# Optimization experiments

Hardware: AMD Instinct MI355X
Metric: run time of the kernel (lower is better)

Reference implementation:

```python
import jax, jax.numpy as jnp
import numpy as np

ALPHA = 0.2  # LeakyReLU negative slope


def setup_inputs() -> dict:
    key = jax.random.key(0)
    k1, k2, k3 = jax.random.split(key, 3)
    B, N, F_IN, F_OUT = 8, 2048, 128, 64
    h = jax.random.normal(k1, (B, N, F_IN), dtype=jnp.float32)
    # nn.Linear(in, out, bias=False).weight is [out, in]; we store the transposed
    # matmul-ready form W: [F_IN, F_OUT].
    W = jax.random.normal(k2, (F_IN, F_OUT), dtype=jnp.float32) * 0.05
    # attn_fc: Linear(2*F_OUT, 1, bias=False) -> weight vector a: [2*F_OUT]
    a = jax.random.normal(k3, (2 * F_OUT,), dtype=jnp.float32) * 0.05
    return {"h": h, "W": W, "a": a}


def reference(h, W, a):
    # h: [B, N, F_in], W: [F_in, F_out], a: [2*F_out]
    F_out = W.shape[1]
    Wh = h @ W  # [B, N, F_out]
    # cat([Wh_i, Wh_j]) @ a == Wh_i @ a1 + Wh_j @ a2 -- identical math,
    # avoids materializing the [B, N, N, 2F] tensor.
    s_i = Wh @ a[:F_out]  # [B, N] contribution of row node i
    s_j = Wh @ a[F_out:]  # [B, N] contribution of col node j
    e = jax.nn.leaky_relu(s_i[:, :, None] + s_j[:, None, :], negative_slope=ALPHA)  # [B, N, N]
    attn = jax.nn.softmax(e, axis=-1)  # softmax over neighbors j
    h_prime = jnp.einsum('bij,bjf->bif', attn, Wh)  # [B, N, F_out]
    return h_prime.mean(axis=1)  # [B, F_out]
```

## Files before the change

### kernel.cpp

```cpp
#include <hip/hip_runtime.h>
#include <hip/hip_bf16.h>


#define B 8
#define N 2048
#define BN (B * N)
#define FIN 128
#define FOUT 64
#define ALPHA 0.2f
#define JS 64
#define SJ (N / JS)

__device__ __forceinline__ float dot4(float4 x, float4 y) {
    return x.x * y.x + x.y * y.y + x.z * y.z + x.w * y.w;
}

__global__ __launch_bounds__(256) void k2_uv(const float* __restrict__ h,
                                             const float* __restrict__ W,
                                             const float* __restrict__ a,
                                             float* __restrict__ u, float* __restrict__ v,
                                             float* __restrict__ out) {
    __shared__ float sa[2 * FOUT];
    __shared__ float sw[2 * FIN];
    int t = threadIdx.x, bid = blockIdx.x;
    if (bid == 0) {
        out[t] = 0.f;
        out[t + 256] = 0.f;
    }
    if (t < 2 * FOUT) sa[t] = a[t];
    __syncthreads();
    {
        int k = t >> 1, half = t & 1;
        float p1 = 0.f, p2 = 0.f;
        #pragma unroll
        for (int i = 0; i < 8; ++i) {
            float4 w4 = *(const float4*)(W + k * FOUT + half * 32 + i * 4);
            float4 a1 = *(const float4*)(sa + half * 32 + i * 4);
            float4 a2 = *(const float4*)(sa + FOUT + half * 32 + i * 4);
            p1 += dot4(w4, a1);
            p2 += dot4(w4, a2);
        }
        p1 += __shfl_xor(p1, 1);
        p2 += __shfl_xor(p2, 1);
        if (half == 0) { sw[k] = p1; sw[FIN + k] = p2; }
    }
    __syncthreads();
    int wave = t >> 6, lane = t & 63;
    int hl = lane & 31;
    const float4 w1x = *(const float4*)(sw + hl * 4);
    const float4 w2x = *(const float4*)(sw + FIN + hl * 4);
    int node0 = bid * 32 + wave * 8;
    #pragma unroll
    for (int it = 0; it < 4; ++it) {
        int node = node0 + it * 2 + (lane >> 5);
        const float4 hx = *(const float4*)(h + (size_t)node * FIN + hl * 4);
        float p1 = dot4(hx, w1x);
        float p2 = dot4(hx, w2x);
        #pragma unroll
        for (int o = 1; o < 32; o <<= 1) {
            p1 += __shfl_xor(p1, o);
            p2 += __shfl_xor(p2, o);
        }
        if (hl == 0) { u[node] = p1; v[node] = p2; }
    }
}

__global__ __launch_bounds__(256) void k3_pass1(const float* __restrict__ u,
                                                const float* __restrict__ v,
                                                float* __restrict__ Ap, float* __restrict__ Bp) {
    __shared__ float sv[SJ], se[SJ], sf[SJ];
    int bid = blockIdx.x;
    int b = bid >> 6, js = bid & 63;
    int t = threadIdx.x;
    if (t < SJ) {
        float vj = v[b * N + js * SJ + t];
        sv[t] = vj;
        se[t] = expf(vj);
        sf[t] = expf(ALPHA * vj);
    }
    __syncthreads();
    float th[8], A[8], Bm[8];
    #pragma unroll
    for (int r = 0; r < 8; ++r) {
        th[r] = -u[b * N + r * 256 + t];
        A[r] = 0.f; Bm[r] = 0.f;
    }
    #pragma unroll
    for (int j = 0; j < SJ; j += 4) {
        float4 vv = *(const float4*)&sv[j];
        float4 ee = *(const float4*)&se[j];
        float4 ff = *(const float4*)&sf[j];
        #pragma unroll
        for (int r = 0; r < 8; ++r) {
            A[r] += (vv.x > th[r]) ? ee.x : 0.f;  Bm[r] += (vv.x > th[r]) ? 0.f : ff.x;
            A[r] += (vv.y > th[r]) ? ee.y : 0.f;  Bm[r] += (vv.y > th[r]) ? 0.f : ff.y;
            A[r] += (vv.z > th[r]) ? ee.z : 0.f;  Bm[r] += (vv.z > th[r]) ? 0.f : ff.z;
            A[r] += (vv.w > th[r]) ? ee.w : 0.f;  Bm[r] += (vv.w > th[r]) ? 0.f : ff.w;
        }
    }
    #pragma unroll
    for (int r = 0; r < 8; ++r) {
        int i = r * 256 + t;
        Ap[js * BN + b * N + i] = A[r];
        Bp[js * BN + b * N + i] = Bm[r];
    }
}

__global__ __launch_bounds__(256) void k4_pass2(const float* __restrict__ u,
                                                const float* __restrict__ v,
                                                const float* __restrict__ Ap,
                                                const float* __restrict__ Bp,
                                                float* __restrict__ cp) {
    __shared__ float spA[256], spB[256];
    __shared__ float su[SJ], sr1[SJ], sr2[SJ];
    int bid = blockIdx.x;
    int b = bid >> 6, is = bid & 63;
    int t = threadIdx.x;
    {
        int n = t & 31, ch = t >> 5;
        int ii0 = b * N + is * 32 + n;
        float pA = 0.f, pB = 0.f;
        #pragma unroll
        for (int s2 = 0; s2 < 8; ++s2) {
            int s = ch * 8 + s2;
            pA += Ap[s * BN + ii0];
            pB += Bp[s * BN + ii0];
        }
        spA[ch * 32 + n] = pA;
        spB[ch * 32 + n] = pB;
    }
    __syncthreads();
    if (t < 32) {
        float As = 0.f, Bs = 0.f;
        #pragma unroll
        for (int ch = 0; ch < 8; ++ch) {
            As += spA[ch * 32 + t];
            Bs += spB[ch * 32 + t];
        }
        float ui = u[b * N + is * 32 + t];
        float eu = expf(ui);
        float fu = expf(ALPHA * ui);
        float inv = 1.0f / (eu * As + fu * Bs);
        su[t] = ui; sr1[t] = eu * inv; sr2[t] = fu * inv;
    }
    __syncthreads();
    float vj[8], th[8], Cn[8], Dn[8];
    #pragma unroll
    for (int r = 0; r < 8; ++r) {
        vj[r] = v[b * N + r * 256 + t];
        th[r] = -vj[r];
        Cn[r] = 0.f; Dn[r] = 0.f;
    }
    #pragma unroll
    for (int i = 0; i < SJ; i += 4) {
        float4 uu = *(const float4*)&su[i];
        float4 r1 = *(const float4*)&sr1[i];
        float4 r2 = *(const float4*)&sr2[i];
        #pragma unroll
        for (int r = 0; r < 8; ++r) {
            Cn[r] += (uu.x > th[r]) ? r1.x : 0.f;  Dn[r] += (uu.x > th[r]) ? 0.f : r2.x;
            Cn[r] += (uu.y > th[r]) ? r1.y : 0.f;  Dn[r] += (uu.y > th[r]) ? 0.f : r2.y;
            Cn[r] += (uu.z > th[r]) ? r1.z : 0.f;  Dn[r] += (uu.z > th[r]) ? 0.f : r2.z;
            Cn[r] += (uu.w > th[r]) ? r1.w : 0.f;  Dn[r] += (uu.w > th[r]) ? 0.f : r2.w;
        }
    }
    #pragma unroll
    for (int r = 0; r < 8; ++r) {
        int j = r * 256 + t;
        cp[is * BN + b * N + j] = expf(vj[r]) * Cn[r] + expf(ALPHA * vj[r]) * Dn[r];
    }
}

__global__ __launch_bounds__(256) void k5_out(const float* __restrict__ h,
                                              const float* __restrict__ W,
                                              const float* __restrict__ cp,
                                              float* __restrict__ out) {
    __shared__ float scp[256];
    __shared__ float sc[32];
    __shared__ float sg2[256];
    __shared__ float sg[128];
    __shared__ float so[256];
    int b = blockIdx.x >> 6, ns = blockIdx.x & 63;
    int t = threadIdx.x;
    {
        int n = t & 31, ch = t >> 5;
        int nn = b * N + ns * 32 + n;
        float c = 0.f;
        #pragma unroll
        for (int s2 = 0; s2 < 8; ++s2) c += cp[(ch * 8 + s2) * BN + nn];
        scp[ch * 32 + n] = c;
    }
    __syncthreads();
    if (t < 32) {
        float c = 0.f;
        #pragma unroll
        for (int ch = 0; ch < 8; ++ch) c += scp[ch * 32 + t];
        sc[t] = c;
    }
    __syncthreads();
    {
        int k = t & 127, half = t >> 7;
        float a0 = 0.f, a1 = 0.f;
        int base = b * N + ns * 32 + half * 16;
        #pragma unroll
        for (int n = 0; n < 16; n += 2) {
            a0 += sc[half * 16 + n]     * h[(size_t)(base + n)     * FIN + k];
            a1 += sc[half * 16 + n + 1] * h[(size_t)(base + n + 1) * FIN + k];
        }
        sg2[half * 128 + k] = a0 + a1;
    }
    __syncthreads();
    if (t < 128) sg[t] = sg2[t] + sg2[128 + t];
    __syncthreads();
    {
        int f = t & 63, q = t >> 6;
        float acc = 0.f;
        #pragma unroll
        for (int kk2 = 0; kk2 < 32; ++kk2) {
            int kk = q * 32 + kk2;
            acc += sg[kk] * W[kk * FOUT + f];
        }
        so[q * 64 + f] = acc;
    }
    __syncthreads();
    if (t < 64) {
        float r = ((so[t] + so[64 + t]) + (so[128 + t] + so[192 + t])) * (1.0f / (float)N);
        atomicAdd(out + b * FOUT + t, r);
    }
}

extern "C" void kernel_launch(void* const* d_in, const int* in_sizes, int n_in,
                              void* d_out, int out_size, void* d_ws, size_t ws_size,
                              hipStream_t stream) {
    const float* h = (const float*)d_in[0];
    const float* W = (const float*)d_in[1];
    const float* a = (const float*)d_in[2];
    float* out = (float*)d_out;

    float* ws = (float*)d_ws;
    float* u  = ws;
    float* v  = u + BN;
    float* Ap = v + BN;
    float* Bp = Ap + JS * BN;
    float* cp = Bp + JS * BN;

    k2_uv<<<512, 256, 0, stream>>>(h, W, a, u, v, out);
    k3_pass1<<<512, 256, 0, stream>>>(u, v, Ap, Bp);
    k4_pass2<<<512, 256, 0, stream>>>(u, v, Ap, Bp, cp);
    k5_out<<<512, 256, 0, stream>>>(h, W, cp, out);
}
```

Before: 84.63 us.

## Fuse four stage kernels into one cooperative kernel with grid syncs

Merges the four separate kernel launches (projection scores, pass1 partial sums, pass2 column coefficients, output reduction) into a single cooperative kernel that separates the stages with grid-wide barriers. The goal is to remove per-launch overhead and inter-kernel gaps. In exchange it depends on all 512 blocks being co-resident (launch bounds allow 2 blocks per SM), and grid.sync adds its own barrier cost. Occupancy limits on register use could also constrain the merged stages.

Result: slower. 249.5 us (+194.9%).

```diff
diff --git a/kernel.cpp b/kernel.cpp
--- a/kernel.cpp
+++ b/kernel.cpp
@@ -1,5 +1,8 @@
 #include <hip/hip_runtime.h>
 #include <hip/hip_bf16.h>
+#include <hip/hip_cooperative_groups.h>
+
+namespace cg = cooperative_groups;
 
 
 #define B 8
@@ -15,217 +18,211 @@
     return x.x * y.x + x.y * y.y + x.z * y.z + x.w * y.w;
 }
 
-__global__ __launch_bounds__(256) void k2_uv(const float* __restrict__ h,
-                                             const float* __restrict__ W,
-                                             const float* __restrict__ a,
-                                             float* __restrict__ u, float* __restrict__ v,
-                                             float* __restrict__ out) {
-    __shared__ float sa[2 * FOUT];
-    __shared__ float sw[2 * FIN];
-    int t = threadIdx.x, bid = blockIdx.x;
-    if (bid == 0) {
-        out[t] = 0.f;
-        out[t + 256] = 0.f;
-    }
-    if (t < 2 * FOUT) sa[t] = a[t];
-    __syncthreads();
-    {
-        int k = t >> 1, half = t & 1;
-        float p1 = 0.f, p2 = 0.f;
-        #pragma unroll
-        for (int i = 0; i < 8; ++i) {
-            float4 w4 = *(const float4*)(W + k * FOUT + half * 32 + i * 4);
-            float4 a1 = *(const float4*)(sa + half * 32 + i * 4);
-            float4 a2 = *(const float4*)(sa + FOUT + half * 32 + i * 4);
-            p1 += dot4(w4, a1);
-            p2 += dot4(w4, a2);
-        }
-        p1 += __shfl_xor(p1, 1);
-        p2 += __shfl_xor(p2, 1);
-        if (half == 0) { sw[k] = p1; sw[FIN + k] = p2; }
-    }
-    __syncthreads();
-    int wave = t >> 6, lane = t & 63;
-    int hl = lane & 31;
-    const float4 w1x = *(const float4*)(sw + hl * 4);
-    const float4 w2x = *(const float4*)(sw + FIN + hl * 4);
-    int node0 = bid * 32 + wave * 8;
-    #pragma unroll
-    for (int it = 0; it < 4; ++it) {
-        int node = node0 + it * 2 + (lane >> 5);
-        const float4 hx = *(const float4*)(h + (size_t)node * FIN + hl * 4);
-        float p1 = dot4(hx, w1x);
-        float p2 = dot4(hx, w2x);
-        #pragma unroll
-        for (int o = 1; o < 32; o <<= 1) {
-            p1 += __shfl_xor(p1, o);
-            p2 += __shfl_xor(p2, o);
-        }
-        if (hl == 0) { u[node] = p1; v[node] = p2; }
-    }
-}
-
-__global__ __launch_bounds__(256) void k3_pass1(const float* __restrict__ u,
-                                                const float* __restrict__ v,
-                                                float* __restrict__ Ap, float* __restrict__ Bp) {
-    __shared__ float sv[SJ], se[SJ], sf[SJ];
-    int bid = blockIdx.x;
-    int b = bid >> 6, js = bid & 63;
-    int t = threadIdx.x;
-    if (t < SJ) {
-        float vj = v[b * N + js * SJ + t];
-        sv[t] = vj;
-        se[t] = expf(vj);
-        sf[t] = expf(ALPHA * vj);
-    }
-    __syncthreads();
-    float th[8], A[8], Bm[8];
-    #pragma unroll
-    for (int r = 0; r < 8; ++r) {
-        th[r] = -u[b * N + r * 256 + t];
-        A[r] = 0.f; Bm[r] = 0.f;
-    }
-    #pragma unroll
-    for (int j = 0; j < SJ; j += 4) {
-        float4 vv = *(const float4*)&sv[j];
-        float4 ee = *(const float4*)&se[j];
-        float4 ff = *(const float4*)&sf[j];
-        #pragma unroll
-        for (int r = 0; r < 8; ++r) {
-            A[r] += (vv.x > th[r]) ? ee.x : 0.f;  Bm[r] += (vv.x > th[r]) ? 0.f : ff.x;
-            A[r] += (vv.y > th[r]) ? ee.y : 0.f;  Bm[r] += (vv.y > th[r]) ? 0.f : ff.y;
-            A[r] += (vv.z > th[r]) ? ee.z : 0.f;  Bm[r] += (vv.z > th[r]) ? 0.f : ff.z;
-            A[r] += (vv.w > th[r]) ? ee.w : 0.f;  Bm[r] += (vv.w > th[r]) ? 0.f : ff.w;
-        }
-    }
-    #pragma unroll
-    for (int r = 0; r < 8; ++r) {
-        int i = r * 256 + t;
-        Ap[js * BN + b * N + i] = A[r];
-        Bp[js * BN + b * N + i] = Bm[r];
-    }
-}
-
-__global__ __launch_bounds__(256) void k4_pass2(const float* __restrict__ u,
-                                                const float* __restrict__ v,
-                                                const float* __restrict__ Ap,
-                                                const float* __restrict__ Bp,
-                                                float* __restrict__ cp) {
-    __shared__ float spA[256], spB[256];
-    __shared__ float su[SJ], sr1[SJ], sr2[SJ];
-    int bid = blockIdx.x;
-    int b = bid >> 6, is = bid & 63;
-    int t = threadIdx.x;
-    {
-        int n = t & 31, ch = t >> 5;
-        int ii0 = b * N + is * 32 + n;
-        float pA = 0.f, pB = 0.f;
-        #pragma unroll
-        for (int s2 = 0; s2 < 8; ++s2) {
-            int s = ch * 8 + s2;
-            pA += Ap[s * BN + ii0];
-            pB += Bp[s * BN + ii0];
-        }
-        spA[ch * 32 + n] = pA;
-        spB[ch * 32 + n] = pB;
-    }
-    __syncthreads();
-    if (t < 32) {
-        float As = 0.f, Bs = 0.f;
-        #pragma unroll
-        for (int ch = 0; ch < 8; ++ch) {
-            As += spA[ch * 32 + t];
-            Bs += spB[ch * 32 + t];
-        }
-        float ui = u[b * N + is * 32 + t];
-        float eu = expf(ui);
-        float fu = expf(ALPHA * ui);
-        float inv = 1.0f / (eu * As + fu * Bs);
-        su[t] = ui; sr1[t] = eu * inv; sr2[t] = fu * inv;
-    }
-    __syncthreads();
-    float vj[8], th[8], Cn[8], Dn[8];
-    #pragma unroll
-    for (int r = 0; r < 8; ++r) {
-        vj[r] = v[b * N + r * 256 + t];
-        th[r] = -vj[r];
-        Cn[r] = 0.f; Dn[r] = 0.f;
-    }
-    #pragma unroll
-    for (int i = 0; i < SJ; i += 4) {
-        float4 uu = *(const float4*)&su[i];
-        float4 r1 = *(const float4*)&sr1[i];
-        float4 r2 = *(const float4*)&sr2[i];
-        #pragma unroll
-        for (int r = 0; r < 8; ++r) {
-            Cn[r] += (uu.x > th[r]) ? r1.x : 0.f;  Dn[r] += (uu.x > th[r]) ? 0.f : r2.x;
-            Cn[r] += (uu.y > th[r]) ? r1.y : 0.f;  Dn[r] += (uu.y > th[r]) ? 0.f : r2.y;
-            Cn[r] += (uu.z > th[r]) ? r1.z : 0.f;  Dn[r] += (uu.z > th[r]) ? 0.f : r2.z;
-            Cn[r] += (uu.w > th[r]) ? r1.w : 0.f;  Dn[r] += (uu.w > th[r]) ? 0.f : r2.w;
-        }
-    }
-    #pragma unroll
-    for (int r = 0; r < 8; ++r) {
-        int j = r * 256 + t;
-        cp[is * BN + b * N + j] = expf(vj[r]) * Cn[r] + expf(ALPHA * vj[r]) * Dn[r];
-    }
-}
-
-__global__ __launch_bounds__(256) void k5_out(const float* __restrict__ h,
-                                              const float* __restrict__ W,
-                                              const float* __restrict__ cp,
-                                              float* __restrict__ out) {
-    __shared__ float scp[256];
-    __shared__ float sc[32];
-    __shared__ float sg2[256];
-    __shared__ float sg[128];
-    __shared__ float so[256];
-    int b = blockIdx.x >> 6, ns = blockIdx.x & 63;
-    int t = threadIdx.x;
-    {
-        int n = t & 31, ch = t >> 5;
-        int nn = b * N + ns * 32 + n;
-        float c = 0.f;
-        #pragma unroll
-        for (int s2 = 0; s2 < 8; ++s2) c += cp[(ch * 8 + s2) * BN + nn];
-        scp[ch * 32 + n] = c;
-    }
-    __syncthreads();
-    if (t < 32) {
-        float c = 0.f;
-        #pragma unroll
-        for (int ch = 0; ch < 8; ++ch) c += scp[ch * 32 + t];
-        sc[t] = c;
-    }
-    __syncthreads();
-    {
-        int k = t & 127, half = t >> 7;
-        float a0 = 0.f, a1 = 0.f;
-        int base = b * N + ns * 32 + half * 16;
-        #pragma unroll
-        for (int n = 0; n < 16; n += 2) {
-            a0 += sc[half * 16 + n]     * h[(size_t)(base + n)     * FIN + k];
-            a1 += sc[half * 16 + n + 1] * h[(size_t)(base + n + 1) * FIN + k];
-        }
-        sg2[half * 128 + k] = a0 + a1;
-    }
-    __syncthreads();
-    if (t < 128) sg[t] = sg2[t] + sg2[128 + t];
-    __syncthreads();
-    {
-        int f = t & 63, q = t >> 6;
-        float acc = 0.f;
-        #pragma unroll
-        for (int kk2 = 0; kk2 < 32; ++kk2) {
-            int kk = q * 32 + kk2;
-            acc += sg[kk] * W[kk * FOUT + f];
-        }
-        so[q * 64 + f] = acc;
-    }
-    __syncthreads();
-    if (t < 64) {
-        float r = ((so[t] + so[64 + t]) + (so[128 + t] + so[192 + t])) * (1.0f / (float)N);
-        atomicAdd(out + b * FOUT + t, r);
+__global__ __launch_bounds__(256, 2) void gat_coop(
+        const float* __restrict__ h, const float* __restrict__ W,
+        const float* __restrict__ a, float* __restrict__ u, float* __restrict__ v,
+        float* __restrict__ Ap, float* __restrict__ Bp, float* __restrict__ cp,
+        float* __restrict__ out) {
+    cg::grid_group grid = cg::this_grid();
+    const int t = threadIdx.x;
+    const int bid = blockIdx.x;
+
+    {
+        __shared__ float sa[2 * FOUT];
+        __shared__ float sw[2 * FIN];
+        if (bid == 0) {
+            out[t] = 0.f;
+            out[t + 256] = 0.f;
+        }
+        if (t < 2 * FOUT) sa[t] = a[t];
+        __syncthreads();
+        {
+            int k = t >> 1, half = t & 1;
+            float p1 = 0.f, p2 = 0.f;
+            #pragma unroll
+            for (int i = 0; i < 8; ++i) {
+                float4 w4 = *(const float4*)(W + k * FOUT + half * 32 + i * 4);
+                float4 a1 = *(const float4*)(sa + half * 32 + i * 4);
+                float4 a2 = *(const float4*)(sa + FOUT + half * 32 + i * 4);
+                p1 += dot4(w4, a1);
+                p2 += dot4(w4, a2);
+            }
+            p1 += __shfl_xor(p1, 1);
+            p2 += __shfl_xor(p2, 1);
+            if (half == 0) { sw[k] = p1; sw[FIN + k] = p2; }
+        }
+        __syncthreads();
+        int wave = t >> 6, lane = t & 63;
+        int hl = lane & 31;
+        const float4 w1x = *(const float4*)(sw + hl * 4);
+        const float4 w2x = *(const float4*)(sw + FIN + hl * 4);
+        int node0 = bid * 32 + wave * 8;
+        #pragma unroll
+        for (int it = 0; it < 4; ++it) {
+            int node = node0 + it * 2 + (lane >> 5);
+            const float4 hx = *(const float4*)(h + (size_t)node * FIN + hl * 4);
+            float p1 = dot4(hx, w1x);
+            float p2 = dot4(hx, w2x);
+            #pragma unroll
+            for (int o = 1; o < 32; o <<= 1) {
+                p1 += __shfl_xor(p1, o);
+                p2 += __shfl_xor(p2, o);
+            }
+            if (hl == 0) { u[node] = p1; v[node] = p2; }
+        }
+    }
+    grid.sync();
+
+    {
+        __shared__ float sv[SJ], se[SJ], sf[SJ];
+        int b = bid >> 6, js = bid & 63;
+        if (t < SJ) {
+            float vj = v[b * N + js * SJ + t];
+            sv[t] = vj;
+            se[t] = expf(vj);
+            sf[t] = expf(ALPHA * vj);
+        }
+        __syncthreads();
+        float th[8], A[8], Bm[8];
+        #pragma unroll
+        for (int r = 0; r < 8; ++r) {
+            th[r] = -u[b * N + r * 256 + t];
+            A[r] = 0.f; Bm[r] = 0.f;
+        }
+        #pragma unroll
+        for (int j = 0; j < SJ; j += 4) {
+            float4 vv = *(const float4*)&sv[j];
+            float4 ee = *(const float4*)&se[j];
+            float4 ff = *(const float4*)&sf[j];
+            #pragma unroll
+            for (int r = 0; r < 8; ++r) {
+                A[r] += (vv.x > th[r]) ? ee.x : 0.f;  Bm[r] += (vv.x > th[r]) ? 0.f : ff.x;
+                A[r] += (vv.y > th[r]) ? ee.y : 0.f;  Bm[r] += (vv.y > th[r]) ? 0.f : ff.y;
+                A[r] += (vv.z > th[r]) ? ee.z : 0.f;  Bm[r] += (vv.z > th[r]) ? 0.f : ff.z;
+                A[r] += (vv.w > th[r]) ? ee.w : 0.f;  Bm[r] += (vv.w > th[r]) ? 0.f : ff.w;
+            }
+        }
+        #pragma unroll
+        for (int r = 0; r < 8; ++r) {
+            int i = r * 256 + t;
+            Ap[js * BN + b * N + i] = A[r];
+            Bp[js * BN + b * N + i] = Bm[r];
+        }
+    }
+    grid.sync();
+
+    {
+        __shared__ float spA[256], spB[256];
+        __shared__ float su[SJ], sr1[SJ], sr2[SJ];
+        int b = bid >> 6, is = bid & 63;
+        {
+            int n = t & 31, ch = t >> 5;
+            int ii0 = b * N + is * 32 + n;
+            float pA = 0.f, pB = 0.f;
+            #pragma unroll
+            for (int s2 = 0; s2 < 8; ++s2) {
+                int s = ch * 8 + s2;
+                pA += Ap[s * BN + ii0];
+                pB += Bp[s * BN + ii0];
+            }
+            spA[ch * 32 + n] = pA;
+            spB[ch * 32 + n] = pB;
+        }
+        __syncthreads();
+        if (t < 32) {
+            float As = 0.f, Bs = 0.f;
+            #pragma unroll
+            for (int ch = 0; ch < 8; ++ch) {
+                As += spA[ch * 32 + t];
+                Bs += spB[ch * 32 + t];
+            }
+            float ui = u[b * N + is * 32 + t];
+            float eu = expf(ui);
+            float fu = expf(ALPHA * ui);
+            float inv = 1.0f / (eu * As + fu * Bs);
+            su[t] = ui; sr1[t] = eu * inv; sr2[t] = fu * inv;
+        }
+        __syncthreads();
+        float vj[8], th[8], Cn[8], Dn[8];
+        #pragma unroll
+        for (int r = 0; r < 8; ++r) {
+            vj[r] = v[b * N + r * 256 + t];
+            th[r] = -vj[r];
+            Cn[r] = 0.f; Dn[r] = 0.f;
+        }
+        #pragma unroll
+        for (int i = 0; i < SJ; i += 4) {
+            float4 uu = *(const float4*)&su[i];
+            float4 r1 = *(const float4*)&sr1[i];
+            float4 r2 = *(const float4*)&sr2[i];
+            #pragma unroll
+            for (int r = 0; r < 8; ++r) {
+                Cn[r] += (uu.x > th[r]) ? r1.x : 0.f;  Dn[r] += (uu.x > th[r]) ? 0.f : r2.x;
+                Cn[r] += (uu.y > th[r]) ? r1.y : 0.f;  Dn[r] += (uu.y > th[r]) ? 0.f : r2.y;
+                Cn[r] += (uu.z > th[r]) ? r1.z : 0.f;  Dn[r] += (uu.z > th[r]) ? 0.f : r2.z;
+                Cn[r] += (uu.w > th[r]) ? r1.w : 0.f;  Dn[r] += (uu.w > th[r]) ? 0.f : r2.w;
+            }
+        }
+        #pragma unroll
+        for (int r = 0; r < 8; ++r) {
+            int j = r * 256 + t;
+            cp[is * BN + b * N + j] = expf(vj[r]) * Cn[r] + expf(ALPHA * vj[r]) * Dn[r];
+        }
+    }
+    grid.sync();
+
+    {
+        __shared__ float scp[256];
+        __shared__ float sc[32];
+        __shared__ float sg2[256];
+        __shared__ float sg[128];
+        __shared__ float so[256];
+        int b = bid >> 6, ns = bid & 63;
+        {
+            int n = t & 31, ch = t >> 5;
+            int nn = b * N + ns * 32 + n;
+            float c = 0.f;
+            #pragma unroll
+            for (int s2 = 0; s2 < 8; ++s2) c += cp[(ch * 8 + s2) * BN + nn];
+            scp[ch * 32 + n] = c;
+        }
+        __syncthreads();
+        if (t < 32) {
+            float c = 0.f;
+            #pragma unroll
+            for (int ch = 0; ch < 8; ++ch) c += scp[ch * 32 + t];
+            sc[t] = c;
+        }
+        __syncthreads();
+        {
+            int k = t & 127, half = t >> 7;
+            float a0 = 0.f, a1 = 0.f;
+            int base = b * N + ns * 32 + half * 16;
+            #pragma unroll
+            for (int n = 0; n < 16; n += 2) {
+                a0 += sc[half * 16 + n]     * h[(size_t)(base + n)     * FIN + k];
+                a1 += sc[half * 16 + n + 1] * h[(size_t)(base + n + 1) * FIN + k];
+            }
+            sg2[half * 128 + k] = a0 + a1;
+        }
+        __syncthreads();
+        if (t < 128) sg[t] = sg2[t] + sg2[128 + t];
+        __syncthreads();
+        {
+            int f = t & 63, q = t >> 6;
+            float acc = 0.f;
+            #pragma unroll
+            for (int kk2 = 0; kk2 < 32; ++kk2) {
+                int kk = q * 32 + kk2;
+                acc += sg[kk] * W[kk * FOUT + f];
+            }
+            so[q * 64 + f] = acc;
+        }
+        __syncthreads();
+        if (t < 64) {
+            float r = ((so[t] + so[64 + t]) + (so[128 + t] + so[192 + t])) * (1.0f / (float)N);
+            atomicAdd(out + b * FOUT + t, r);
+        }
     }
 }
 
@@ -244,8 +241,7 @@
     float* Bp = Ap + JS * BN;
     float* cp = Bp + JS * BN;
 
-    k2_uv<<<512, 256, 0, stream>>>(h, W, a, u, v, out);
-    k3_pass1<<<512, 256, 0, stream>>>(u, v, Ap, Bp);
-    k4_pass2<<<512, 256, 0, stream>>>(u, v, Ap, Bp, cp);
-    k5_out<<<512, 256, 0, stream>>>(h, W, cp, out);
+    void* args[] = {(void*)&h, (void*)&W, (void*)&a, (void*)&u, (void*)&v,
+                    (void*)&Ap, (void*)&Bp, (void*)&cp, (void*)&out};
+    hipLaunchCooperativeKernel((void*)gat_coop, dim3(512), dim3(256), args, 0, stream);
 }
```
